# Optimization experiments

Measured on AMD Instinct MI355X. Metric: run time of the kernel, lower is better.

The kernel has to match this reference:

```python
import jax, jax.numpy as jnp
import numpy as np
import math

B, S, E, H, D = 2, 2048, 1024, 16, 64

def setup_inputs() -> dict:
    key = jax.random.key(0)
    ks = jax.random.split(key, 9)
    sc = 0.02
    return {
        "x": jax.random.normal(ks[0], (B, S, E), jnp.float32),
        "Wq": jax.random.normal(ks[1], (H, E, D), jnp.float32) * sc,
        "Wk": jax.random.normal(ks[2], (H, E, D), jnp.float32) * sc,
        "Wv": jax.random.normal(ks[3], (H, E, D), jnp.float32) * sc,
        "bq": jax.random.normal(ks[4], (H, D), jnp.float32) * sc,
        "bk": jax.random.normal(ks[5], (H, D), jnp.float32) * sc,
        "bv": jax.random.normal(ks[6], (H, D), jnp.float32) * sc,
        "Wo": jax.random.normal(ks[7], (H * D, E), jnp.float32) * sc,
        "bo": jax.random.normal(ks[8], (E,), jnp.float32) * sc,
    }

def reference(x, Wq, Wk, Wv, bq, bk, bv, Wo, bo):
    # per-head projections, batched over heads: [B,H,S,D]
    q = jnp.einsum('bse,hed->bhsd', x, Wq) + bq[None, :, None, :]
    k = jnp.einsum('bse,hed->bhsd', x, Wk) + bk[None, :, None, :]
    v = jnp.einsum('bse,hed->bhsd', x, Wv) + bv[None, :, None, :]
    # full score matrix [B,H,S,S], scaled by sqrt(head_size) as in original
    scores = jnp.einsum('bhqd,bhkd->bhqk', q, k) / math.sqrt(D)
    causal = jnp.tril(jnp.ones((S, S), bool))  # tril mask as in buffer
    scores = jnp.where(causal[None, None], scores, -jnp.inf)
    attn = jax.nn.softmax(scores, axis=-1)
    out = jnp.einsum('bhqk,bhkd->bhqd', attn, v)
    # concat heads in head order: [B,S,H*D]
    out = out.transpose(0, 2, 1, 3).reshape(B, S, H * D)
    # output projection (dropout is identity in eval / p=0)
    return out @ Wo + bo
```

## Files before the change

### kernel.cpp

```cpp
#include <hip/hip_runtime.h>

#define BB 2
#define SS 2048
#define EE 1024
#define HH 16
#define DD 64

typedef unsigned short u16;
typedef float f4 __attribute__((ext_vector_type(4)));
typedef __bf16 b8 __attribute__((ext_vector_type(8)));
typedef short s8i __attribute__((ext_vector_type(8)));
typedef u16 u16x4 __attribute__((ext_vector_type(4)));

__device__ inline u16 f2b(float f) {
  unsigned u = __builtin_bit_cast(unsigned, f);
  unsigned r = (u + 0x7fffu + ((u >> 16) & 1u)) >> 16;
  return (u16)r;
}

__global__ __launch_bounds__(256) void prep(const float* __restrict__ x,
                                            const float* __restrict__ Wq,
                                            const float* __restrict__ Wk,
                                            const float* __restrict__ Wv,
                                            const float* __restrict__ Wo,
                                            u16* __restrict__ xb,
                                            u16* __restrict__ Wt,
                                            u16* __restrict__ Wot) {
  int bid = blockIdx.x;
  int t = threadIdx.x;
  if (bid < 1024) {
    int i0 = bid * 256 + t;
    for (int j = 0; j < 4; ++j) {
      int i = i0 + j * 262144;
      f4 v = ((const f4*)x)[i];
      u16x4 o;
      for (int k2 = 0; k2 < 4; ++k2) o[k2] = f2b(v[k2]);
      ((u16x4*)xb)[i] = o;
    }
  } else if (bid < 1792) {
    __shared__ float tile[64][65];
    int z = bid - 1024;
    int y = z >> 4;
    int e0 = (z & 15) * 64;
    int qkv = y >> 4, h = y & 15;
    const float* W = (qkv == 0) ? Wq : (qkv == 1) ? Wk : Wv;
    for (int p = 0; p < 16; ++p) {
      int i = p * 4 + (t >> 6), d = t & 63;
      tile[i][d] = W[((size_t)h * EE + e0 + i) * DD + d];
    }
    __syncthreads();
    for (int p = 0; p < 16; ++p) {
      int d = p * 4 + (t >> 6), i = t & 63;
      Wt[((size_t)qkv * 1024 + h * 64 + d) * EE + e0 + i] = f2b(tile[i][d]);
    }
  } else {
    __shared__ float tile2[64][65];
    int z = bid - 1792;
    int e0 = (z & 15) * 64, c0 = (z >> 4) * 64;
    for (int p = 0; p < 16; ++p) {
      int i = p * 4 + (t >> 6), j = t & 63;
      tile2[i][j] = Wo[(size_t)(e0 + i) * (HH * DD) + c0 + j];
    }
    __syncthreads();
    for (int p = 0; p < 16; ++p) {
      int j = p * 4 + (t >> 6), i = t & 63;
      Wot[(size_t)(c0 + j) * EE + e0 + i] = f2b(tile2[i][j]);
    }
  }
}

template <int MODE>
__global__ __launch_bounds__(256) void gemm128(
    const u16* __restrict__ A, const u16* __restrict__ Bm,
    u16* __restrict__ Qo, u16* __restrict__ Ko, u16* __restrict__ Vo,
    const float* __restrict__ bq, const float* __restrict__ bk,
    const float* __restrict__ bv,
    float* __restrict__ Co, const float* __restrict__ bo) {
  const int K = 1024;
  __shared__ u16 As[128 * 32];
  __shared__ u16 Bs[128 * 32];
  int t = threadIdx.x;
  int lane = t & 63, w = t >> 6;
  int wr = w >> 1, wc = w & 1;
  int lr = lane & 15, lg = lane >> 4;
  int m0 = blockIdx.y * 128, n0 = blockIdx.x * 128;

  f4 acc[4][4];
  const f4 z4 = {0.f, 0.f, 0.f, 0.f};
  for (int mi = 0; mi < 4; ++mi)
    for (int ni = 0; ni < 4; ++ni) acc[mi][ni] = z4;

  int r0 = t >> 2, s0 = t & 3;
  const u16* ga0 = A + (size_t)(m0 + r0) * K + s0 * 8;
  const u16* gb0 = Bm + (size_t)(n0 + r0) * K + s0 * 8;
  u16* la0 = As + w * 512;
  u16* la1 = As + 2048 + w * 512;
  u16* lb0 = Bs + w * 512;
  u16* lb1 = Bs + 2048 + w * 512;

  for (int ks = 0; ks < K / 32; ++ks) {
    int k0 = ks * 32;
    __builtin_amdgcn_global_load_lds(
        (const __attribute__((address_space(1))) void*)(ga0 + k0),
        (__attribute__((address_space(3))) void*)la0, 16, 0, 0);
    __builtin_amdgcn_global_load_lds(
        (const __attribute__((address_space(1))) void*)(ga0 + 64 * K + k0),
        (__attribute__((address_space(3))) void*)la1, 16, 0, 0);
    __builtin_amdgcn_global_load_lds(
        (const __attribute__((address_space(1))) void*)(gb0 + k0),
        (__attribute__((address_space(3))) void*)lb0, 16, 0, 0);
    __builtin_amdgcn_global_load_lds(
        (const __attribute__((address_space(1))) void*)(gb0 + 64 * K + k0),
        (__attribute__((address_space(3))) void*)lb1, 16, 0, 0);
    __syncthreads();
    b8 af[4], bf[4];
    for (int mi = 0; mi < 4; ++mi)
      af[mi] = *(const b8*)&As[(wr * 64 + mi * 16 + lr) * 32 + lg * 8];
    for (int ni = 0; ni < 4; ++ni)
      bf[ni] = *(const b8*)&Bs[(wc * 64 + ni * 16 + lr) * 32 + lg * 8];
    for (int mi = 0; mi < 4; ++mi)
      for (int ni = 0; ni < 4; ++ni)
        acc[mi][ni] = __builtin_amdgcn_mfma_f32_16x16x32_bf16(af[mi], bf[ni],
                                                              acc[mi][ni], 0, 0, 0);
    __syncthreads();
  }

  const float QSC = 0.18033688011112042f;
  for (int mi = 0; mi < 4; ++mi)
    for (int ni = 0; ni < 4; ++ni)
      for (int r = 0; r < 4; ++r) {
        int m_g = m0 + wr * 64 + mi * 16 + lg * 4 + r;
        int n_g = n0 + wc * 64 + ni * 16 + lr;
        float v = acc[mi][ni][r];
        if (MODE == 0) {
          int qkv = n_g >> 10, hd = n_g & 1023;
          const float* bias = (qkv == 0) ? bq : (qkv == 1) ? bk : bv;
          v += bias[hd];
          int b = m_g >> 11, s = m_g & 2047;
          int h = hd >> 6, d = hd & 63;
          if (qkv == 0) {
            Qo[(((size_t)b * HH + h) * SS + s) * DD + d] = f2b(v * QSC);
          } else if (qkv == 1) {
            Ko[(((size_t)b * HH + h) * SS + s) * DD + d] = f2b(v);
          } else {
            Vo[(((size_t)b * HH + h) * DD + d) * SS + s] = f2b(v);
          }
        } else {
          Co[(size_t)m_g * 1024 + n_g] = v + bo[n_g];
        }
      }
}

#define KST 72
#define PST 72
__global__ __launch_bounds__(256) void fattn(const u16* __restrict__ Qb,
                                             const u16* __restrict__ Kb,
                                             const u16* __restrict__ VTb,
                                             u16* __restrict__ AO) {
  __shared__ u16 Kl[2][64 * KST];
  __shared__ u16 Vl[2][64 * KST];
  __shared__ u16 Pl[4][16 * PST];

  int t = threadIdx.x, lane = t & 63, w = t >> 6;
  int lr = lane & 15, lg = lane >> 4;
  int bh = blockIdx.y;
  int b = bh >> 4, h = bh & 15;
  size_t base = (size_t)bh * SS * DD;

  int r0 = t >> 2, s0 = t & 3;
  u16* kl0 = &Kl[0][r0 * KST + s0 * 8];
  u16* kl1 = &Kl[1][r0 * KST + s0 * 8];
  u16* vl0 = &Vl[0][r0 * KST + s0 * 8];
  u16* vl1 = &Vl[1][r0 * KST + s0 * 8];
  const u16* kg = Kb + base + (size_t)r0 * DD + s0 * 8;
  const u16* vg = VTb + base + (size_t)r0 * SS + s0 * 8;

  for (int half = 0; half < 2; ++half) {
    int qt = half ? blockIdx.x : 31 - blockIdx.x;
    int qbase = qt * 64;
    int nt = qt + 1;

    const u16* qp = Qb + base + (size_t)(qbase + w * 16 + lr) * DD;
    b8 qf0 = *(const b8*)(qp + lg * 8);
    b8 qf1 = *(const b8*)(qp + 32 + lg * 8);

    const f4 z4 = {0.f, 0.f, 0.f, 0.f};
    f4 o[4];
    for (int i = 0; i < 4; ++i) o[i] = z4;
    float mrow[4], lsum[4];
    for (int r = 0; r < 4; ++r) { mrow[r] = -1e30f; lsum[r] = 0.f; }
    int qg = qbase + w * 16 + lg * 4;

    {
      *(s8i*)kl0 = *(const s8i*)(kg);
      *(s8i*)(kl0 + 32) = *(const s8i*)(kg + 32);
      *(s8i*)vl0 = *(const s8i*)(vg);
      *(s8i*)(vl0 + 32) = *(const s8i*)(vg + 32);
    }
    __syncthreads();

    for (int kt = 0; kt < nt; ++kt) {
      int cur = kt & 1;
      int kv0 = kt * 64;

      s8i nk0, nk1, nv0, nv1;
      bool more = (kt + 1 < nt);
      if (more) {
        const u16* kgn = kg + (size_t)(kv0 + 64) * DD;
        const u16* vgn = vg + kv0 + 64;
        nk0 = *(const s8i*)(kgn);
        nk1 = *(const s8i*)(kgn + 32);
        nv0 = *(const s8i*)(vgn);
        nv1 = *(const s8i*)(vgn + 32);
      }

      f4 sa[4];
      for (int n = 0; n < 4; ++n) sa[n] = z4;
      for (int n = 0; n < 4; ++n) {
        b8 kf0 = *(const b8*)&Kl[cur][(n * 16 + lr) * KST + lg * 8];
        b8 kf1 = *(const b8*)&Kl[cur][(n * 16 + lr) * KST + 32 + lg * 8];
        sa[n] = __builtin_amdgcn_mfma_f32_16x16x32_bf16(qf0, kf0, sa[n], 0, 0, 0);
        sa[n] = __builtin_amdgcn_mfma_f32_16x16x32_bf16(qf1, kf1, sa[n], 0, 0, 0);
      }

      if (kt == nt - 1) {
        for (int r = 0; r < 4; ++r) {
          int q = qg + r;
          if (kv0 + lr > q) sa[0][r] = -1e30f;
          if (kv0 + 16 + lr > q) sa[1][r] = -1e30f;
          if (kv0 + 32 + lr > q) sa[2][r] = -1e30f;
          if (kv0 + 48 + lr > q) sa[3][r] = -1e30f;
        }
      }

      float scl[4];
      for (int r = 0; r < 4; ++r) {
        float mx = fmaxf(fmaxf(sa[0][r], sa[1][r]), fmaxf(sa[2][r], sa[3][r]));
        mx = fmaxf(mx, __shfl_xor(mx, 1));
        mx = fmaxf(mx, __shfl_xor(mx, 2));
        mx = fmaxf(mx, __shfl_xor(mx, 4));
        mx = fmaxf(mx, __shfl_xor(mx, 8));
        float mn = fmaxf(mrow[r], mx);
        float sc = __builtin_amdgcn_exp2f(mrow[r] - mn);
        float p0 = __builtin_amdgcn_exp2f(sa[0][r] - mn);
        float p1 = __builtin_amdgcn_exp2f(sa[1][r] - mn);
        float p2 = __builtin_amdgcn_exp2f(sa[2][r] - mn);
        float p3 = __builtin_amdgcn_exp2f(sa[3][r] - mn);
        lsum[r] = lsum[r] * sc + ((p0 + p1) + (p2 + p3));
        mrow[r] = mn;
        scl[r] = sc;
        int prow = (lg * 4 + r) * PST;
        Pl[w][prow + lr] = f2b(p0);
        Pl[w][prow + 16 + lr] = f2b(p1);
        Pl[w][prow + 32 + lr] = f2b(p2);
        Pl[w][prow + 48 + lr] = f2b(p3);
      }
      for (int n = 0; n < 4; ++n) {
        f4 ov = o[n];
        for (int r = 0; r < 4; ++r) ov[r] *= scl[r];
        o[n] = ov;
      }

      b8 pf0 = *(const b8*)&Pl[w][lr * PST + lg * 8];
      b8 pf1 = *(const b8*)&Pl[w][lr * PST + 32 + lg * 8];
      for (int n = 0; n < 4; ++n) {
        b8 vf0 = *(const b8*)&Vl[cur][(n * 16 + lr) * KST + lg * 8];
        b8 vf1 = *(const b8*)&Vl[cur][(n * 16 + lr) * KST + 32 + lg * 8];
        o[n] = __builtin_amdgcn_mfma_f32_16x16x32_bf16(pf0, vf0, o[n], 0, 0, 0);
        o[n] = __builtin_amdgcn_mfma_f32_16x16x32_bf16(pf1, vf1, o[n], 0, 0, 0);
      }

      if (more) {
        u16* kln = cur ? kl0 : kl1;
        u16* vln = cur ? vl0 : vl1;
        *(s8i*)kln = nk0;
        *(s8i*)(kln + 32) = nk1;
        *(s8i*)vln = nv0;
        *(s8i*)(vln + 32) = nv1;
      }
      __syncthreads();
    }

    float rl[4];
    for (int r = 0; r < 4; ++r) {
      float s = lsum[r];
      s += __shfl_xor(s, 1);
      s += __shfl_xor(s, 2);
      s += __shfl_xor(s, 4);
      s += __shfl_xor(s, 8);
      rl[r] = 1.f / s;
    }
    for (int n = 0; n < 4; ++n)
      for (int r = 0; r < 4; ++r) {
        int qgr = qg + r;
        int d = n * 16 + lr;
        AO[((size_t)b * SS + qgr) * (HH * DD) + h * DD + d] = f2b(o[n][r] * rl[r]);
      }
    __syncthreads();
  }
}

extern "C" void kernel_launch(void* const* d_in, const int* in_sizes, int n_in,
                              void* d_out, int out_size, void* d_ws, size_t ws_size,
                              hipStream_t stream) {
  const float* x  = (const float*)d_in[0];
  const float* Wq = (const float*)d_in[1];
  const float* Wk = (const float*)d_in[2];
  const float* Wv = (const float*)d_in[3];
  const float* bq = (const float*)d_in[4];
  const float* bk = (const float*)d_in[5];
  const float* bv = (const float*)d_in[6];
  const float* Wo = (const float*)d_in[7];
  const float* bo = (const float*)d_in[8];

  char* ws = (char*)d_ws;
  u16* xb  = (u16*)(ws);
  u16* Wt  = (u16*)(ws + ((size_t)8 << 20));
  u16* Wot = (u16*)(ws + ((size_t)14 << 20));
  u16* Qw  = (u16*)(ws + ((size_t)16 << 20));
  u16* Kw  = (u16*)(ws + ((size_t)24 << 20));
  u16* VTw = (u16*)(ws + ((size_t)32 << 20));
  u16* AO  = xb;

  prep<<<2048, 256, 0, stream>>>(x, Wq, Wk, Wv, Wo, xb, Wt, Wot);
  gemm128<0><<<dim3(24, 32), 256, 0, stream>>>(xb, Wt, Qw, Kw, VTw, bq, bk, bv,
                                               nullptr, nullptr);
  fattn<<<dim3(16, 32), 256, 0, stream>>>(Qw, Kw, VTw, AO);
  gemm128<1><<<dim3(8, 32), 256, 0, stream>>>(AO, Wot, nullptr, nullptr, nullptr,
                                              nullptr, nullptr, nullptr,
                                              (float*)d_out, bo);
}
```

Before: 221.3 us.

## Split attention work into one q-tile per block and narrow output GEMM tiles

The attention kernel now launches one block per query tile (1024 blocks) instead of pairing a long and a short causal tile in each block, with a diagonal swizzle so heavy and light tiles spread across the grid. The output projection gets its own kernel with 128x64 tiles, doubling its block count from 256 to 512 so more of the GPU's compute units stay busy. Both changes target underutilisation from too few blocks. In exchange, causal load balance now depends on the hardware scheduler rather than the explicit pairing, and the narrower GEMM tiles reuse less data per block.

Result: slower. 238.5 us (+7.8%).

```diff
diff --git a/kernel.cpp b/kernel.cpp
--- a/kernel.cpp
+++ b/kernel.cpp
@@ -69,13 +69,11 @@
   }
 }
 
-template <int MODE>
-__global__ __launch_bounds__(256) void gemm128(
+__global__ __launch_bounds__(256) void gemmQKV(
     const u16* __restrict__ A, const u16* __restrict__ Bm,
     u16* __restrict__ Qo, u16* __restrict__ Ko, u16* __restrict__ Vo,
     const float* __restrict__ bq, const float* __restrict__ bk,
-    const float* __restrict__ bv,
-    float* __restrict__ Co, const float* __restrict__ bo) {
+    const float* __restrict__ bv) {
   const int K = 1024;
   __shared__ u16 As[128 * 32];
   __shared__ u16 Bs[128 * 32];
@@ -132,22 +130,75 @@
         int m_g = m0 + wr * 64 + mi * 16 + lg * 4 + r;
         int n_g = n0 + wc * 64 + ni * 16 + lr;
         float v = acc[mi][ni][r];
-        if (MODE == 0) {
-          int qkv = n_g >> 10, hd = n_g & 1023;
-          const float* bias = (qkv == 0) ? bq : (qkv == 1) ? bk : bv;
-          v += bias[hd];
-          int b = m_g >> 11, s = m_g & 2047;
-          int h = hd >> 6, d = hd & 63;
-          if (qkv == 0) {
-            Qo[(((size_t)b * HH + h) * SS + s) * DD + d] = f2b(v * QSC);
-          } else if (qkv == 1) {
-            Ko[(((size_t)b * HH + h) * SS + s) * DD + d] = f2b(v);
-          } else {
-            Vo[(((size_t)b * HH + h) * DD + d) * SS + s] = f2b(v);
-          }
+        int qkv = n_g >> 10, hd = n_g & 1023;
+        const float* bias = (qkv == 0) ? bq : (qkv == 1) ? bk : bv;
+        v += bias[hd];
+        int b = m_g >> 11, s = m_g & 2047;
+        int h = hd >> 6, d = hd & 63;
+        if (qkv == 0) {
+          Qo[(((size_t)b * HH + h) * SS + s) * DD + d] = f2b(v * QSC);
+        } else if (qkv == 1) {
+          Ko[(((size_t)b * HH + h) * SS + s) * DD + d] = f2b(v);
         } else {
-          Co[(size_t)m_g * 1024 + n_g] = v + bo[n_g];
+          Vo[(((size_t)b * HH + h) * DD + d) * SS + s] = f2b(v);
         }
+      }
+}
+
+__global__ __launch_bounds__(256) void gemmO(const u16* __restrict__ A,
+                                             const u16* __restrict__ Bm,
+                                             float* __restrict__ Co,
+                                             const float* __restrict__ bo) {
+  const int K = 1024;
+  __shared__ u16 As[128 * 32];
+  __shared__ u16 Bs[64 * 32];
+  int t = threadIdx.x;
+  int lane = t & 63, w = t >> 6;
+  int lr = lane & 15, lg = lane >> 4;
+  int m0 = blockIdx.y * 128, n0 = blockIdx.x * 64;
+
+  f4 acc[2][4];
+  const f4 z4 = {0.f, 0.f, 0.f, 0.f};
+  for (int mi = 0; mi < 2; ++mi)
+    for (int ni = 0; ni < 4; ++ni) acc[mi][ni] = z4;
+
+  int r0 = t >> 2, s0 = t & 3;
+  const u16* ga0 = A + (size_t)(m0 + r0) * K + s0 * 8;
+  const u16* gb0 = Bm + (size_t)(n0 + r0) * K + s0 * 8;
+  u16* la0 = As + w * 512;
+  u16* la1 = As + 2048 + w * 512;
+  u16* lb0 = Bs + w * 512;
+
+  for (int ks = 0; ks < K / 32; ++ks) {
+    int k0 = ks * 32;
+    __builtin_amdgcn_global_load_lds(
+        (const __attribute__((address_space(1))) void*)(ga0 + k0),
+        (__attribute__((address_space(3))) void*)la0, 16, 0, 0);
+    __builtin_amdgcn_global_load_lds(
+        (const __attribute__((address_space(1))) void*)(ga0 + 64 * K + k0),
+        (__attribute__((address_space(3))) void*)la1, 16, 0, 0);
+    __builtin_amdgcn_global_load_lds(
+        (const __attribute__((address_space(1))) void*)(gb0 + k0),
+        (__attribute__((address_space(3))) void*)lb0, 16, 0, 0);
+    __syncthreads();
+    b8 af[2], bf[4];
+    for (int mi = 0; mi < 2; ++mi)
+      af[mi] = *(const b8*)&As[(w * 32 + mi * 16 + lr) * 32 + lg * 8];
+    for (int ni = 0; ni < 4; ++ni)
+      bf[ni] = *(const b8*)&Bs[(ni * 16 + lr) * 32 + lg * 8];
+    for (int mi = 0; mi < 2; ++mi)
+      for (int ni = 0; ni < 4; ++ni)
+        acc[mi][ni] = __builtin_amdgcn_mfma_f32_16x16x32_bf16(af[mi], bf[ni],
+                                                              acc[mi][ni], 0, 0, 0);
+    __syncthreads();
+  }
+
+  for (int mi = 0; mi < 2; ++mi)
+    for (int ni = 0; ni < 4; ++ni)
+      for (int r = 0; r < 4; ++r) {
+        int m_g = m0 + w * 32 + mi * 16 + lg * 4 + r;
+        int n_g = n0 + ni * 16 + lr;
+        Co[(size_t)m_g * 1024 + n_g] = acc[mi][ni][r] + bo[n_g];
       }
 }
 
@@ -163,7 +214,9 @@
 
   int t = threadIdx.x, lane = t & 63, w = t >> 6;
   int lr = lane & 15, lg = lane >> 4;
-  int bh = blockIdx.y;
+  int bx = blockIdx.x, by = blockIdx.y;
+  int qt = 31 - ((bx + by) & 31);
+  int bh = by;
   int b = bh >> 4, h = bh & 15;
   size_t base = (size_t)bh * SS * DD;
 
@@ -175,129 +228,125 @@
   const u16* kg = Kb + base + (size_t)r0 * DD + s0 * 8;
   const u16* vg = VTb + base + (size_t)r0 * SS + s0 * 8;
 
-  for (int half = 0; half < 2; ++half) {
-    int qt = half ? blockIdx.x : 31 - blockIdx.x;
-    int qbase = qt * 64;
-    int nt = qt + 1;
-
-    const u16* qp = Qb + base + (size_t)(qbase + w * 16 + lr) * DD;
-    b8 qf0 = *(const b8*)(qp + lg * 8);
-    b8 qf1 = *(const b8*)(qp + 32 + lg * 8);
-
-    const f4 z4 = {0.f, 0.f, 0.f, 0.f};
-    f4 o[4];
-    for (int i = 0; i < 4; ++i) o[i] = z4;
-    float mrow[4], lsum[4];
-    for (int r = 0; r < 4; ++r) { mrow[r] = -1e30f; lsum[r] = 0.f; }
-    int qg = qbase + w * 16 + lg * 4;
-
-    {
-      *(s8i*)kl0 = *(const s8i*)(kg);
-      *(s8i*)(kl0 + 32) = *(const s8i*)(kg + 32);
-      *(s8i*)vl0 = *(const s8i*)(vg);
-      *(s8i*)(vl0 + 32) = *(const s8i*)(vg + 32);
-    }
-    __syncthreads();
-
-    for (int kt = 0; kt < nt; ++kt) {
-      int cur = kt & 1;
-      int kv0 = kt * 64;
-
-      s8i nk0, nk1, nv0, nv1;
-      bool more = (kt + 1 < nt);
-      if (more) {
-        const u16* kgn = kg + (size_t)(kv0 + 64) * DD;
-        const u16* vgn = vg + kv0 + 64;
-        nk0 = *(const s8i*)(kgn);
-        nk1 = *(const s8i*)(kgn + 32);
-        nv0 = *(const s8i*)(vgn);
-        nv1 = *(const s8i*)(vgn + 32);
+  int qbase = qt * 64;
+  int nt = qt + 1;
+
+  const u16* qp = Qb + base + (size_t)(qbase + w * 16 + lr) * DD;
+  b8 qf0 = *(const b8*)(qp + lg * 8);
+  b8 qf1 = *(const b8*)(qp + 32 + lg * 8);
+
+  const f4 z4 = {0.f, 0.f, 0.f, 0.f};
+  f4 o[4];
+  for (int i = 0; i < 4; ++i) o[i] = z4;
+  float mrow[4], lsum[4];
+  for (int r = 0; r < 4; ++r) { mrow[r] = -1e30f; lsum[r] = 0.f; }
+  int qg = qbase + w * 16 + lg * 4;
+
+  {
+    *(s8i*)kl0 = *(const s8i*)(kg);
+    *(s8i*)(kl0 + 32) = *(const s8i*)(kg + 32);
+    *(s8i*)vl0 = *(const s8i*)(vg);
+    *(s8i*)(vl0 + 32) = *(const s8i*)(vg + 32);
+  }
+  __syncthreads();
+
+  for (int kt = 0; kt < nt; ++kt) {
+    int cur = kt & 1;
+    int kv0 = kt * 64;
+
+    s8i nk0, nk1, nv0, nv1;
+    bool more = (kt + 1 < nt);
+    if (more) {
+      const u16* kgn = kg + (size_t)(kv0 + 64) * DD;
+      const u16* vgn = vg + kv0 + 64;
+      nk0 = *(const s8i*)(kgn);
+      nk1 = *(const s8i*)(kgn + 32);
+      nv0 = *(const s8i*)(vgn);
+      nv1 = *(const s8i*)(vgn + 32);
+    }
+
+    f4 sa[4];
+    for (int n = 0; n < 4; ++n) sa[n] = z4;
+    for (int n = 0; n < 4; ++n) {
+      b8 kf0 = *(const b8*)&Kl[cur][(n * 16 + lr) * KST + lg * 8];
+      b8 kf1 = *(const b8*)&Kl[cur][(n * 16 + lr) * KST + 32 + lg * 8];
+      sa[n] = __builtin_amdgcn_mfma_f32_16x16x32_bf16(qf0, kf0, sa[n], 0, 0, 0);
+      sa[n] = __builtin_amdgcn_mfma_f32_16x16x32_bf16(qf1, kf1, sa[n], 0, 0, 0);
+    }
+
+    if (kt == nt - 1) {
+      for (int r = 0; r < 4; ++r) {
+        int q = qg + r;
+        if (kv0 + lr > q) sa[0][r] = -1e30f;
+        if (kv0 + 16 + lr > q) sa[1][r] = -1e30f;
+        if (kv0 + 32 + lr > q) sa[2][r] = -1e30f;
+        if (kv0 + 48 + lr > q) sa[3][r] = -1e30f;
       }
-
-      f4 sa[4];
-      for (int n = 0; n < 4; ++n) sa[n] = z4;
-      for (int n = 0; n < 4; ++n) {
-        b8 kf0 = *(const b8*)&Kl[cur][(n * 16 + lr) * KST + lg * 8];
-        b8 kf1 = *(const b8*)&Kl[cur][(n * 16 + lr) * KST + 32 + lg * 8];
-        sa[n] = __builtin_amdgcn_mfma_f32_16x16x32_bf16(qf0, kf0, sa[n], 0, 0, 0);
-        sa[n] = __builtin_amdgcn_mfma_f32_16x16x32_bf16(qf1, kf1, sa[n], 0, 0, 0);
-      }
-
-      if (kt == nt - 1) {
-        for (int r = 0; r < 4; ++r) {
-          int q = qg + r;
-          if (kv0 + lr > q) sa[0][r] = -1e30f;
-          if (kv0 + 16 + lr > q) sa[1][r] = -1e30f;
-          if (kv0 + 32 + lr > q) sa[2][r] = -1e30f;
-          if (kv0 + 48 + lr > q) sa[3][r] = -1e30f;
-        }
-      }
-
-      float scl[4];
-      for (int r = 0; r < 4; ++r) {
-        float mx = fmaxf(fmaxf(sa[0][r], sa[1][r]), fmaxf(sa[2][r], sa[3][r]));
-        mx = fmaxf(mx, __shfl_xor(mx, 1));
-        mx = fmaxf(mx, __shfl_xor(mx, 2));
-        mx = fmaxf(mx, __shfl_xor(mx, 4));
-        mx = fmaxf(mx, __shfl_xor(mx, 8));
-        float mn = fmaxf(mrow[r], mx);
-        float sc = __builtin_amdgcn_exp2f(mrow[r] - mn);
-        float p0 = __builtin_amdgcn_exp2f(sa[0][r] - mn);
-        float p1 = __builtin_amdgcn_exp2f(sa[1][r] - mn);
-        float p2 = __builtin_amdgcn_exp2f(sa[2][r] - mn);
-        float p3 = __builtin_amdgcn_exp2f(sa[3][r] - mn);
-        lsum[r] = lsum[r] * sc + ((p0 + p1) + (p2 + p3));
-        mrow[r] = mn;
-        scl[r] = sc;
-        int prow = (lg * 4 + r) * PST;
-        Pl[w][prow + lr] = f2b(p0);
-        Pl[w][prow + 16 + lr] = f2b(p1);
-        Pl[w][prow + 32 + lr] = f2b(p2);
-        Pl[w][prow + 48 + lr] = f2b(p3);
-      }
-      for (int n = 0; n < 4; ++n) {
-        f4 ov = o[n];
-        for (int r = 0; r < 4; ++r) ov[r] *= scl[r];
-        o[n] = ov;
-      }
-
-      b8 pf0 = *(const b8*)&Pl[w][lr * PST + lg * 8];
-      b8 pf1 = *(const b8*)&Pl[w][lr * PST + 32 + lg * 8];
-      for (int n = 0; n < 4; ++n) {
-        b8 vf0 = *(const b8*)&Vl[cur][(n * 16 + lr) * KST + lg * 8];
-        b8 vf1 = *(const b8*)&Vl[cur][(n * 16 + lr) * KST + 32 + lg * 8];
-        o[n] = __builtin_amdgcn_mfma_f32_16x16x32_bf16(pf0, vf0, o[n], 0, 0, 0);
-        o[n] = __builtin_amdgcn_mfma_f32_16x16x32_bf16(pf1, vf1, o[n], 0, 0, 0);
-      }
-
-      if (more) {
-        u16* kln = cur ? kl0 : kl1;
-        u16* vln = cur ? vl0 : vl1;
-        *(s8i*)kln = nk0;
-        *(s8i*)(kln + 32) = nk1;
-        *(s8i*)vln = nv0;
-        *(s8i*)(vln + 32) = nv1;
-      }
-      __syncthreads();
-    }
-
-    float rl[4];
+    }
+
+    float scl[4];
     for (int r = 0; r < 4; ++r) {
-      float s = lsum[r];
-      s += __shfl_xor(s, 1);
-      s += __shfl_xor(s, 2);
-      s += __shfl_xor(s, 4);
-      s += __shfl_xor(s, 8);
-      rl[r] = 1.f / s;
-    }
-    for (int n = 0; n < 4; ++n)
-      for (int r = 0; r < 4; ++r) {
-        int qgr = qg + r;
-        int d = n * 16 + lr;
-        AO[((size_t)b * SS + qgr) * (HH * DD) + h * DD + d] = f2b(o[n][r] * rl[r]);
-      }
-    __syncthreads();
-  }
+      float mx = fmaxf(fmaxf(sa[0][r], sa[1][r]), fmaxf(sa[2][r], sa[3][r]));
+      mx = fmaxf(mx, __shfl_xor(mx, 1));
+      mx = fmaxf(mx, __shfl_xor(mx, 2));
+      mx = fmaxf(mx, __shfl_xor(mx, 4));
+      mx = fmaxf(mx, __shfl_xor(mx, 8));
+      float mn = fmaxf(mrow[r], mx);
+      float sc = __builtin_amdgcn_exp2f(mrow[r] - mn);
+      float p0 = __builtin_amdgcn_exp2f(sa[0][r] - mn);
+      float p1 = __builtin_amdgcn_exp2f(sa[1][r] - mn);
+      float p2 = __builtin_amdgcn_exp2f(sa[2][r] - mn);
+      float p3 = __builtin_amdgcn_exp2f(sa[3][r] - mn);
+      lsum[r] = lsum[r] * sc + ((p0 + p1) + (p2 + p3));
+      mrow[r] = mn;
+      scl[r] = sc;
+      int prow = (lg * 4 + r) * PST;
+      Pl[w][prow + lr] = f2b(p0);
+      Pl[w][prow + 16 + lr] = f2b(p1);
+      Pl[w][prow + 32 + lr] = f2b(p2);
+      Pl[w][prow + 48 + lr] = f2b(p3);
+    }
+    for (int n = 0; n < 4; ++n) {
+      f4 ov = o[n];
+      for (int r = 0; r < 4; ++r) ov[r] *= scl[r];
+      o[n] = ov;
+    }
+
+    b8 pf0 = *(const b8*)&Pl[w][lr * PST + lg * 8];
+    b8 pf1 = *(const b8*)&Pl[w][lr * PST + 32 + lg * 8];
+    for (int n = 0; n < 4; ++n) {
+      b8 vf0 = *(const b8*)&Vl[cur][(n * 16 + lr) * KST + lg * 8];
+      b8 vf1 = *(const b8*)&Vl[cur][(n * 16 + lr) * KST + 32 + lg * 8];
+      o[n] = __builtin_amdgcn_mfma_f32_16x16x32_bf16(pf0, vf0, o[n], 0, 0, 0);
+      o[n] = __builtin_amdgcn_mfma_f32_16x16x32_bf16(pf1, vf1, o[n], 0, 0, 0);
+    }
+
+    if (more) {
+      u16* kln = cur ? kl0 : kl1;
+      u16* vln = cur ? vl0 : vl1;
+      *(s8i*)kln = nk0;
+      *(s8i*)(kln + 32) = nk1;
+      *(s8i*)vln = nv0;
+      *(s8i*)(vln + 32) = nv1;
+    }
+    __syncthreads();
+  }
+
+  float rl[4];
+  for (int r = 0; r < 4; ++r) {
+    float s = lsum[r];
+    s += __shfl_xor(s, 1);
+    s += __shfl_xor(s, 2);
+    s += __shfl_xor(s, 4);
+    s += __shfl_xor(s, 8);
+    rl[r] = 1.f / s;
+  }
+  for (int n = 0; n < 4; ++n)
+    for (int r = 0; r < 4; ++r) {
+      int qgr = qg + r;
+      int d = n * 16 + lr;
+      AO[((size_t)b * SS + qgr) * (HH * DD) + h * DD + d] = f2b(o[n][r] * rl[r]);
+    }
 }
 
 extern "C" void kernel_launch(void* const* d_in, const int* in_sizes, int n_in,
@@ -323,10 +372,7 @@
   u16* AO  = xb;
 
   prep<<<2048, 256, 0, stream>>>(x, Wq, Wk, Wv, Wo, xb, Wt, Wot);
-  gemm128<0><<<dim3(24, 32), 256, 0, stream>>>(xb, Wt, Qw, Kw, VTw, bq, bk, bv,
-                                               nullptr, nullptr);
-  fattn<<<dim3(16, 32), 256, 0, stream>>>(Qw, Kw, VTw, AO);
-  gemm128<1><<<dim3(8, 32), 256, 0, stream>>>(AO, Wot, nullptr, nullptr, nullptr,
-                                              nullptr, nullptr, nullptr,
-                                              (float*)d_out, bo);
-}
+  gemmQKV<<<dim3(24, 32), 256, 0, stream>>>(xb, Wt, Qw, Kw, VTw, bq, bk, bv);
+  fattn<<<dim3(32, 32), 256, 0, stream>>>(Qw, Kw, VTw, AO);
+  gemmO<<<dim3(16, 32), 256, 0, stream>>>(AO, Wot, (float*)d_out, bo);
+}
```
